# Kernel optimization log

Hardware: AMD Instinct MI355X
Metric: run time of the kernel (lower is better)

Reference implementation:

```python
import jax, jax.numpy as jnp
import numpy as np

B, N, K = 64, 1024, 16  # graphs per batch, nodes per graph, top-k (k=16 hardcoded in module)
EPS = 1e-20


def setup_inputs() -> dict:
    key = jax.random.key(0)
    ks = jax.random.split(key, 6)
    C = 128
    x = jax.random.normal(ks[0], (B * N, C), jnp.float32)
    pos = jax.random.normal(ks[1], (B * N, 3), jnp.float32)
    W1 = jax.random.normal(ks[2], (C, C), jnp.float32) / np.sqrt(C).astype(np.float32)
    b1 = jnp.zeros((C,), jnp.float32)
    gamma = jnp.ones((C,), jnp.float32)
    beta = jnp.zeros((C,), jnp.float32)
    W2 = jax.random.normal(ks[3], (C, 10), jnp.float32) / np.sqrt(C).astype(np.float32)
    b2 = jnp.zeros((10,), jnp.float32)
    t = jnp.ones((1,), jnp.float32)
    return dict(x=x, pos=pos, W1=W1, b1=b1, gamma=gamma, beta=beta, W2=W2, b2=b2, t=t)


def _edge_arrays(idx):
    # idx: (B, N, K) per-target top-k source node indices (graph-local)
    offs = (jnp.arange(B, dtype=jnp.int32) * N)[:, None, None]
    src = (idx + offs).reshape(-1)
    tgt = (jnp.broadcast_to(jnp.arange(N, dtype=jnp.int32)[None, :, None], (B, N, K)) + offs).reshape(-1)
    return jnp.stack([src, tgt])  # (2, B*N*K)


def _knn_edges(pos):
    # KNNGraph(k=16) on positions, loop=False (exclude self)
    p = pos.reshape(B, N, 3)
    d2 = jnp.sum((p[:, :, None, :] - p[:, None, :, :]) ** 2, axis=-1)  # (B,N,N)
    d2 = d2 + jnp.eye(N, dtype=d2.dtype) * 1e10
    _, idx = jax.lax.top_k(-d2, K)  # nearest K per node
    return _edge_arrays(idx)


def reference(x, pos, W1, b1, gamma, beta, W2, b2, t):
    key = jax.random.key(42)
    k1, k2 = jax.random.split(key)
    # tg MLP: lin -> batchnorm -> relu -> lin (training-mode batch stats over nodes)
    h = x @ W1 + b1
    mu = h.mean(axis=0)
    var = h.var(axis=0)
    h = (h - mu) / jnp.sqrt(var + 1e-5) * gamma + beta
    h = jax.nn.relu(h)
    emb = h @ W2 + b2  # (B*N, 10)
    emb = emb + jax.random.uniform(k1, emb.shape, emb.dtype) * 0.001
    e = emb.reshape(B, N, 10)
    # pairwise distances per graph (vectorized over the python loop in the original)
    diff = e[:, :, None, :] - e[:, None, :, :]  # (B,N,N,10)
    dist = jnp.linalg.norm(diff, axis=-1)  # (B,N,N)
    p = jnp.exp(-t[0] * dist ** 2)
    u = jax.random.uniform(k2, p.shape, p.dtype)
    gumbel = -jnp.log(-jnp.log(u + EPS) + EPS)
    noisy_logits = jnp.log(p + EPS) + gumbel
    # torch topk over dim=0 (sources) for each target column -> transpose then top_k on last axis
    vals, idx = jax.lax.top_k(jnp.swapaxes(noisy_logits, 1, 2), K)  # (B,N,K)
    vals = jax.nn.softmax(vals, axis=-1)
    vals = vals / vals.max(axis=-1, keepdims=True)
    soft_idx = _edge_arrays(idx)  # (2, B*N*K)
    knn_idx = _knn_edges(pos)
    edge_index = jnp.concatenate([soft_idx, knn_idx], axis=1)
    return vals.reshape(-1), soft_idx, edge_index
```

## Files before the change

### kernel.cpp

```cpp
#include <hip/hip_runtime.h>
#include <stdint.h>
#include <math.h>

#define BG 64
#define NG 1024
#define KK 16
#define CC 128
#define NNODE (BG * NG)
#define NSOFT (BG * NG * KK)
#define FEPS 1e-20f

__host__ __device__ __forceinline__ uint32_t rotl32u(uint32_t x, int r) {
  return (x << r) | (x >> (32 - r));
}

__host__ __device__ __forceinline__ void tf2x32(uint32_t k0, uint32_t k1,
                                                uint32_t x0, uint32_t x1,
                                                uint32_t &o0, uint32_t &o1) {
  uint32_t k2 = k0 ^ k1 ^ 0x1BD11BDAu;
  x0 += k0; x1 += k1;
#define TFR(r) { x0 += x1; x1 = rotl32u(x1, r); x1 ^= x0; }
  TFR(13) TFR(15) TFR(26) TFR(6)
  x0 += k1; x1 += k2 + 1u;
  TFR(17) TFR(29) TFR(16) TFR(24)
  x0 += k2; x1 += k0 + 2u;
  TFR(13) TFR(15) TFR(26) TFR(6)
  x0 += k0; x1 += k1 + 3u;
  TFR(17) TFR(29) TFR(16) TFR(24)
  x0 += k1; x1 += k2 + 4u;
  TFR(13) TFR(15) TFR(26) TFR(6)
  x0 += k2; x1 += k0 + 5u;
#undef TFR
  o0 = x0; o1 = x1;
}

__device__ __forceinline__ float jax_uniform01(uint32_t ka, uint32_t kb, uint32_t m) {
  uint32_t o0, o1;
  tf2x32(ka, kb, 0u, m, o0, o1);
  uint32_t bits = o0 ^ o1;
  float f = __uint_as_float((bits >> 9) | 0x3f800000u) - 1.0f;
  return fmaxf(f, 0.0f);
}

#define LDS_WAIT() asm volatile("s_waitcnt lgkmcnt(0)" ::: "memory")

__global__ __launch_bounds__(256) void k_gemm1(const float* __restrict__ x,
                                               const float* __restrict__ W1,
                                               const float* __restrict__ b1,
                                               float* __restrict__ h,
                                               float* __restrict__ p1,
                                               float* __restrict__ p2) {
  __shared__ __align__(16) float xs[64 * 128];
  const int t = threadIdx.x;
  const size_t blockBase = (size_t)blockIdx.x * (64 * 128);
  #pragma unroll
  for (int j = 0; j < 32; ++j) xs[t + j * 256] = x[blockBase + t + j * 256];
  __syncthreads();
  const int c = t & 127;
  const int rg = t >> 7;
  float acc[32];
  #pragma unroll
  for (int j = 0; j < 32; ++j) acc[j] = 0.f;
  const float* xrow = &xs[rg * 32 * 128];
  for (int k4 = 0; k4 < 128; k4 += 4) {
    const float w0 = W1[(size_t)(k4 + 0) * 128 + c];
    const float w1 = W1[(size_t)(k4 + 1) * 128 + c];
    const float w2 = W1[(size_t)(k4 + 2) * 128 + c];
    const float w3 = W1[(size_t)(k4 + 3) * 128 + c];
    #pragma unroll
    for (int j = 0; j < 32; ++j) {
      const float4 xv = *(const float4*)&xrow[j * 128 + k4];
      acc[j] = fmaf(xv.x, w0, acc[j]);
      acc[j] = fmaf(xv.y, w1, acc[j]);
      acc[j] = fmaf(xv.z, w2, acc[j]);
      acc[j] = fmaf(xv.w, w3, acc[j]);
    }
  }
  const float bb = b1[c];
  float s1 = 0.f, s2 = 0.f;
  #pragma unroll
  for (int j = 0; j < 32; ++j) {
    const float v = acc[j] + bb;
    h[blockBase + (size_t)(rg * 32 + j) * 128 + c] = v;
    s1 += v;
    s2 = fmaf(v, v, s2);
  }
  __syncthreads();
  float* r1 = xs;
  float* r2 = xs + 256;
  r1[rg * 128 + c] = s1;
  r2[rg * 128 + c] = s2;
  __syncthreads();
  if (t < 128) {
    p1[(size_t)t * 1024 + blockIdx.x] = r1[t] + r1[128 + t];
  } else {
    const int cc = t - 128;
    p2[(size_t)cc * 1024 + blockIdx.x] = r2[cc] + r2[128 + cc];
  }
}

__global__ __launch_bounds__(256) void k_bn_final(const float* __restrict__ p1,
                                                  const float* __restrict__ p2,
                                                  const float* __restrict__ gamma,
                                                  const float* __restrict__ beta,
                                                  float* __restrict__ scale,
                                                  float* __restrict__ shift) {
  const int c = blockIdx.x, t = threadIdx.x;
  const float* q1 = p1 + (size_t)c * 1024;
  const float* q2 = p2 + (size_t)c * 1024;
  float a1 = q1[t] + q1[t + 256] + q1[t + 512] + q1[t + 768];
  float a2 = q2[t] + q2[t + 256] + q2[t + 512] + q2[t + 768];
  __shared__ float r1[256], r2[256];
  r1[t] = a1; r2[t] = a2;
  __syncthreads();
  for (int o = 128; o > 0; o >>= 1) {
    if (t < o) { r1[t] += r1[t + o]; r2[t] += r2[t + o]; }
    __syncthreads();
  }
  if (t == 0) {
    const float mu = r1[0] * (1.0f / NNODE);
    float var = r2[0] * (1.0f / NNODE) - mu * mu;
    var = fmaxf(var, 0.f);
    const float sc = gamma[c] / sqrtf(var + 1e-5f);
    scale[c] = sc;
    shift[c] = beta[c] - mu * sc;
  }
}

__global__ __launch_bounds__(256) void k_emb(const float* __restrict__ h,
                                             const float* __restrict__ scale,
                                             const float* __restrict__ shift,
                                             const float* __restrict__ W2,
                                             const float* __restrict__ b2,
                                             float* __restrict__ e,
                                             uint32_t ka, uint32_t kb) {
  __shared__ __align__(16) float hn[64 * 132];
  const int t = threadIdx.x;
  const int rowBase = blockIdx.x * 64;
  {
    const int c = t & 127;
    const float sc = scale[c], sh = shift[c];
    #pragma unroll
    for (int j = 0; j < 32; ++j) {
      const int r = (t >> 7) + j * 2;
      const float v = fmaf(h[(size_t)(rowBase + r) * 128 + c], sc, sh);
      hn[r * 132 + c] = fmaxf(v, 0.f);
    }
  }
  __syncthreads();
  #pragma unroll
  for (int j = 0; j < 3; ++j) {
    const int o = t + j * 256;
    if (o < 640) {
      const int r = o / 10;
      const int col = o - r * 10;
      float acc = 0.f;
      for (int k4 = 0; k4 < 128; k4 += 4) {
        const float4 hv = *(const float4*)&hn[r * 132 + k4];
        acc = fmaf(hv.x, W2[(k4 + 0) * 10 + col], acc);
        acc = fmaf(hv.y, W2[(k4 + 1) * 10 + col], acc);
        acc = fmaf(hv.z, W2[(k4 + 2) * 10 + col], acc);
        acc = fmaf(hv.w, W2[(k4 + 3) * 10 + col], acc);
      }
      acc += b2[col];
      const uint32_t m = (uint32_t)(rowBase + r) * 10u + (uint32_t)col;
      const float u = jax_uniform01(ka, kb, m);
      e[(size_t)(rowBase + r) * 10 + col] = acc + u * 0.001f;
    }
  }
}

__global__ __launch_bounds__(1024, 4) void k_soft(const float* __restrict__ e,
                                                  const float* __restrict__ tsc,
                                                  float* __restrict__ out,
                                                  uint32_t ka, uint32_t kb) {
  __shared__ __align__(16) float2 els2[5 * NG];
  __shared__ float    cv[16][48];
  __shared__ int      cidx[16][48];
  __shared__ uint32_t cnt[16];
  __shared__ float    o16v[16][16];
  __shared__ int      o16i[16][16];

  const int t = threadIdx.x, lane = t & 63, w = t >> 6;
  const int node = blockIdx.x * 16 + w;
  const int b = blockIdx.x >> 6;
  const int jt = node & (NG - 1);
  const float negt = -tsc[0];
  const float* eg = e + (size_t)b * (NG * 10);

  if (lane == 0) cnt[w] = 0u;

  {
    const int s = t;
    const float2* rp = (const float2*)(eg + (size_t)s * 10);
    els2[0 * NG + s] = rp[0];
    els2[1 * NG + s] = rp[1];
    els2[2 * NG + s] = rp[2];
    els2[3 * NG + s] = rp[3];
    els2[4 * NG + s] = rp[4];
  }
  __syncthreads();

  float ej[10];
  #pragma unroll
  for (int p = 0; p < 5; ++p) {
    const float2 a = els2[p * NG + jt];
    ej[2 * p] = a.x; ej[2 * p + 1] = a.y;
  }

  float vv[16];
  const uint32_t mL = ((uint32_t)b << 20) + ((uint32_t)lane << 10) + (uint32_t)jt;
  const uint32_t kxa = ka, kxb = kb;
  const uint32_t kxc = ka ^ kb ^ 0x1BD11BDAu;

#define DIST(ACC, S) { \
    const float2 r0 = els2[0 * NG + (S)]; \
    const float2 r1 = els2[1 * NG + (S)]; \
    const float2 r2 = els2[2 * NG + (S)]; \
    const float2 r3 = els2[3 * NG + (S)]; \
    const float2 r4 = els2[4 * NG + (S)]; \
    float dd; \
    dd = ej[0] - r0.x; ACC = dd * dd; \
    dd = ej[1] - r0.y; ACC = fmaf(dd, dd, ACC); \
    dd = ej[2] - r1.x; ACC = fmaf(dd, dd, ACC); \
    dd = ej[3] - r1.y; ACC = fmaf(dd, dd, ACC); \
    dd = ej[4] - r2.x; ACC = fmaf(dd, dd, ACC); \
    dd = ej[5] - r2.y; ACC = fmaf(dd, dd, ACC); \
    dd = ej[6] - r3.x; ACC = fmaf(dd, dd, ACC); \
    dd = ej[7] - r3.y; ACC = fmaf(dd, dd, ACC); \
    dd = ej[8] - r4.x; ACC = fmaf(dd, dd, ACC); \
    dd = ej[9] - r4.y; ACC = fmaf(dd, dd, ACC); }

#define TFR4(r) { \
    xA0 += xA1; xA1 = rotl32u(xA1, r); xA1 ^= xA0; \
    xB0 += xB1; xB1 = rotl32u(xB1, r); xB1 ^= xB0; \
    xC0 += xC1; xC1 = rotl32u(xC1, r); xC1 ^= xC0; \
    xD0 += xD1; xD1 = rotl32u(xD1, r); xD1 ^= xD0; }
#define INJ4(A, B) { \
    xA0 += (A); xA1 += (B); \
    xB0 += (A); xB1 += (B); \
    xC0 += (A); xC1 += (B); \
    xD0 += (A); xD1 += (B); }

#define TAIL(ACC, X0, X1, ST) { \
    const uint32_t bits = (X0) ^ (X1); \
    float uu = __uint_as_float((bits >> 9) | 0x3f800000u) - 1.0f; \
    uu = fmaxf(uu, 0.0f); \
    const float dist = sqrtf(ACC); \
    const float d2 = dist * dist; \
    const float p = __expf(negt * d2); \
    const float li = __logf(uu + FEPS); \
    const float g = -__logf(FEPS - li); \
    vv[ST] = __logf(p + FEPS) + g; }

  #pragma unroll
  for (int g4 = 0; g4 < 4; ++g4) {
    const int sA = (g4 * 4 + 0) * 64 + lane;
    const int sB = (g4 * 4 + 1) * 64 + lane;
    const int sC = (g4 * 4 + 2) * 64 + lane;
    const int sD = (g4 * 4 + 3) * 64 + lane;
    float aA, aB, aC, aD;
    DIST(aA, sA)
    DIST(aB, sB)
    DIST(aC, sC)
    DIST(aD, sD)
    uint32_t xA0 = kxa, xA1 = (mL + (uint32_t)((g4 * 4 + 0) << 16)) + kxb;
    uint32_t xB0 = kxa, xB1 = (mL + (uint32_t)((g4 * 4 + 1) << 16)) + kxb;
    uint32_t xC0 = kxa, xC1 = (mL + (uint32_t)((g4 * 4 + 2) << 16)) + kxb;
    uint32_t xD0 = kxa, xD1 = (mL + (uint32_t)((g4 * 4 + 3) << 16)) + kxb;
    TFR4(13) TFR4(15) TFR4(26) TFR4(6)
    INJ4(kxb, kxc + 1u)
    TFR4(17) TFR4(29) TFR4(16) TFR4(24)
    INJ4(kxc, kxa + 2u)
    TFR4(13) TFR4(15) TFR4(26) TFR4(6)
    INJ4(kxa, kxb + 3u)
    TFR4(17) TFR4(29) TFR4(16) TFR4(24)
    INJ4(kxb, kxc + 4u)
    TFR4(13) TFR4(15) TFR4(26) TFR4(6)
    INJ4(kxc, kxa + 5u)
    TAIL(aA, xA0, xA1, g4 * 4 + 0)
    TAIL(aB, xB0, xB1, g4 * 4 + 1)
    TAIL(aC, xC0, xC1, g4 * 4 + 2)
    TAIL(aD, xD0, xD1, g4 * 4 + 3)
  }
#undef DIST
#undef TFR4
#undef INJ4
#undef TAIL

  float lo = -51.0f, hi = 17.0f;
  #pragma unroll 1
  for (int it = 0; it < 24; ++it) {
    const float mid = 0.5f * (lo + hi);
    int c = 0;
    #pragma unroll
    for (int st = 0; st < 16; ++st)
      c += (int)__popcll(__ballot(vv[st] >= mid));
    if (c >= 16) lo = mid; else hi = mid;
  }
  const float tau = lo;

  #pragma unroll
  for (int st = 0; st < 16; ++st) {
    if (vv[st] >= tau) {
      const uint32_t pos = atomicAdd(&cnt[w], 1u);
      if (pos < 48u) { cv[w][pos] = vv[st]; cidx[w][pos] = st * 64 + lane; }
    }
  }
  LDS_WAIT();

  int C = (int)cnt[w]; if (C > 48) C = 48;
  const float mvv = (lane < C) ? cv[w][lane] : 0.f;
  const int   mii = (lane < C) ? cidx[w][lane] : 0;
  int rank = 0;
  for (int j = 0; j < C; ++j) {
    const float vj = cv[w][j];
    const int ij = cidx[w][j];
    if (vj > mvv || (vj == mvv && ij < mii)) ++rank;
  }
  if (lane < C && rank < 16) { o16v[w][rank] = mvv; o16i[w][rank] = mii; }
  LDS_WAIT();

  if (lane < 16) {
    const float vq = o16v[w][lane];
    const float m0 = o16v[w][0];
    float uex = __expf(vq - m0);
    float ss = uex;
    #pragma unroll
    for (int off = 1; off < 16; off <<= 1) ss += __shfl_xor(ss, off, 16);
    const float u0 = __shfl(uex, 0, 16);
    const float s0v = u0 / ss;
    const float sv = uex / ss;
    const float o = sv / s0v;
    const size_t base = (size_t)node * KK + lane;
    const float tgtf = (float)node;
    const float srcf = (float)(b * NG + o16i[w][lane]);
    out[base] = o;
    out[(size_t)NSOFT + base] = srcf;
    out[2 * (size_t)NSOFT + base] = tgtf;
    out[3 * (size_t)NSOFT + base] = srcf;
    out[5 * (size_t)NSOFT + base] = tgtf;
  }
}

__global__ __launch_bounds__(1024, 4) void k_knn(const float* __restrict__ pos,
                                                 float* __restrict__ out) {
  __shared__ float    pls[3 * NG];
  __shared__ float    cv[16][48];
  __shared__ int      cidx[16][48];
  __shared__ uint32_t cnt[16];
  __shared__ int      o16i[16][16];

  const int t = threadIdx.x, lane = t & 63, w = t >> 6;
  const int node = blockIdx.x * 16 + w;
  const int b = blockIdx.x >> 6;
  const int it = node & (NG - 1);
  const float* pg = pos + (size_t)b * (NG * 3);

  if (lane == 0) cnt[w] = 0u;

  for (int f = t; f < 3072; f += 1024) {
    const int r = f / 3, d = f - r * 3;
    pls[d * NG + r] = pg[f];
  }
  __syncthreads();

  const float px = pls[0 * NG + it];
  const float py = pls[1 * NG + it];
  const float pz = pls[2 * NG + it];

  float vv[16];
  #pragma unroll
  for (int st = 0; st < 16; ++st) {
    const int s = st * 64 + lane;
    const float dx = px - pls[0 * NG + s];
    const float dy = py - pls[1 * NG + s];
    const float dz = pz - pls[2 * NG + s];
    float d2 = dx * dx;
    d2 = fmaf(dy, dy, d2);
    d2 = fmaf(dz, dz, d2);
    if (s == it) d2 += 1e10f;
    vv[st] = -d2;
  }

  float lo = -70.0f, hi = 1.0f;
  #pragma unroll 1
  for (int bs = 0; bs < 26; ++bs) {
    const float mid = 0.5f * (lo + hi);
    int c = 0;
    #pragma unroll
    for (int st = 0; st < 16; ++st)
      c += (int)__popcll(__ballot(vv[st] >= mid));
    if (c >= 16) lo = mid; else hi = mid;
  }
  const float tau = lo;

  #pragma unroll
  for (int st = 0; st < 16; ++st) {
    if (vv[st] >= tau) {
      const uint32_t pos = atomicAdd(&cnt[w], 1u);
      if (pos < 48u) { cv[w][pos] = vv[st]; cidx[w][pos] = st * 64 + lane; }
    }
  }
  LDS_WAIT();

  int C = (int)cnt[w]; if (C > 48) C = 48;
  const float mvv = (lane < C) ? cv[w][lane] : 0.f;
  const int   mii = (lane < C) ? cidx[w][lane] : 0;
  int rank = 0;
  for (int j = 0; j < C; ++j) {
    const float vj = cv[w][j];
    const int ij = cidx[w][j];
    if (vj > mvv || (vj == mvv && ij < mii)) ++rank;
  }
  if (lane < C && rank < 16) o16i[w][rank] = mii;
  LDS_WAIT();

  if (lane < 16) {
    const size_t base = (size_t)node * KK + lane;
    out[4 * (size_t)NSOFT + base] = (float)(b * NG + o16i[w][lane]);
    out[6 * (size_t)NSOFT + base] = (float)node;
  }
}

extern "C" void kernel_launch(void* const* d_in, const int* in_sizes, int n_in,
                              void* d_out, int out_size, void* d_ws, size_t ws_size,
                              hipStream_t stream) {
  const float* x     = (const float*)d_in[0];
  const float* pos   = (const float*)d_in[1];
  const float* W1    = (const float*)d_in[2];
  const float* b1    = (const float*)d_in[3];
  const float* gamma = (const float*)d_in[4];
  const float* beta  = (const float*)d_in[5];
  const float* W2    = (const float*)d_in[6];
  const float* b2    = (const float*)d_in[7];
  const float* t     = (const float*)d_in[8];
  float* out = (float*)d_out;

  float* ws    = (float*)d_ws;
  float* h     = ws;
  float* e     = h + (size_t)NNODE * CC;
  float* p1    = e + (size_t)NNODE * 10;
  float* p2    = p1 + 128 * 1024;
  float* scale = p2 + 128 * 1024;
  float* shift = scale + CC;

  uint32_t k1a, k1b, k2a, k2b;
  tf2x32(0u, 42u, 0u, 0u, k1a, k1b);
  tf2x32(0u, 42u, 0u, 1u, k2a, k2b);

  k_gemm1<<<dim3(NNODE / 64), dim3(256), 0, stream>>>(x, W1, b1, h, p1, p2);
  k_bn_final<<<dim3(CC), dim3(256), 0, stream>>>(p1, p2, gamma, beta, scale, shift);
  k_emb<<<dim3(NNODE / 64), dim3(256), 0, stream>>>(h, scale, shift, W2, b2, e, k1a, k1b);
  k_knn<<<dim3(NNODE / 16), dim3(1024), 0, stream>>>(pos, out);
  k_soft<<<dim3(NNODE / 16), dim3(1024), 0, stream>>>(e, t, out, k2a, k2b);
}
```

Measured before the change: 488.7 us.

## Store embeddings planar and read them from global/L2 instead of LDS in k_soft

```diff
diff --git a/kernel.cpp b/kernel.cpp
--- a/kernel.cpp
+++ b/kernel.cpp
@@ -132,9 +132,10 @@
                                              const float* __restrict__ shift,
                                              const float* __restrict__ W2,
                                              const float* __restrict__ b2,
-                                             float* __restrict__ e,
+                                             float2* __restrict__ et2,
                                              uint32_t ka, uint32_t kb) {
   __shared__ __align__(16) float hn[64 * 132];
+  __shared__ float et[64 * 10];
   const int t = threadIdx.x;
   const int rowBase = blockIdx.x * 64;
   {
@@ -165,46 +166,41 @@
       acc += b2[col];
       const uint32_t m = (uint32_t)(rowBase + r) * 10u + (uint32_t)col;
       const float u = jax_uniform01(ka, kb, m);
-      e[(size_t)(rowBase + r) * 10 + col] = acc + u * 0.001f;
+      et[r * 10 + col] = acc + u * 0.001f;
     }
   }
-}
-
-__global__ __launch_bounds__(1024, 4) void k_soft(const float* __restrict__ e,
-                                                  const float* __restrict__ tsc,
-                                                  float* __restrict__ out,
-                                                  uint32_t ka, uint32_t kb) {
-  __shared__ __align__(16) float2 els2[5 * NG];
-  __shared__ float    cv[16][48];
-  __shared__ int      cidx[16][48];
-  __shared__ uint32_t cnt[16];
-  __shared__ float    o16v[16][16];
-  __shared__ int      o16i[16][16];
+  __syncthreads();
+  if (t < 320) {
+    const int r = t & 63, p = t >> 6;
+    et2[(size_t)p * NNODE + rowBase + r] =
+        make_float2(et[r * 10 + 2 * p], et[r * 10 + 2 * p + 1]);
+  }
+}
+
+__global__ __launch_bounds__(256, 4) void k_soft(const float2* __restrict__ et2,
+                                                 const float* __restrict__ tsc,
+                                                 float* __restrict__ out,
+                                                 uint32_t ka, uint32_t kb) {
+  __shared__ float    cv[4][48];
+  __shared__ int      cidx[4][48];
+  __shared__ uint32_t cnt[4];
+  __shared__ float    o16v[4][16];
+  __shared__ int      o16i[4][16];
 
   const int t = threadIdx.x, lane = t & 63, w = t >> 6;
-  const int node = blockIdx.x * 16 + w;
-  const int b = blockIdx.x >> 6;
+  const int node = blockIdx.x * 4 + w;
+  const int b = node >> 10;
   const int jt = node & (NG - 1);
+  const int gb = b << 10;
   const float negt = -tsc[0];
-  const float* eg = e + (size_t)b * (NG * 10);
 
   if (lane == 0) cnt[w] = 0u;
-
-  {
-    const int s = t;
-    const float2* rp = (const float2*)(eg + (size_t)s * 10);
-    els2[0 * NG + s] = rp[0];
-    els2[1 * NG + s] = rp[1];
-    els2[2 * NG + s] = rp[2];
-    els2[3 * NG + s] = rp[3];
-    els2[4 * NG + s] = rp[4];
-  }
-  __syncthreads();
+  LDS_WAIT();
 
   float ej[10];
   #pragma unroll
   for (int p = 0; p < 5; ++p) {
-    const float2 a = els2[p * NG + jt];
+    const float2 a = et2[(size_t)p * NNODE + node];
     ej[2 * p] = a.x; ej[2 * p + 1] = a.y;
   }
 
@@ -214,11 +210,11 @@
   const uint32_t kxc = ka ^ kb ^ 0x1BD11BDAu;
 
 #define DIST(ACC, S) { \
-    const float2 r0 = els2[0 * NG + (S)]; \
-    const float2 r1 = els2[1 * NG + (S)]; \
-    const float2 r2 = els2[2 * NG + (S)]; \
-    const float2 r3 = els2[3 * NG + (S)]; \
-    const float2 r4 = els2[4 * NG + (S)]; \
+    const float2 r0 = et2[0 * (size_t)NNODE + gb + (S)]; \
+    const float2 r1 = et2[1 * (size_t)NNODE + gb + (S)]; \
+    const float2 r2 = et2[2 * (size_t)NNODE + gb + (S)]; \
+    const float2 r3 = et2[3 * (size_t)NNODE + gb + (S)]; \
+    const float2 r4 = et2[4 * (size_t)NNODE + gb + (S)]; \
     float dd; \
     dd = ej[0] - r0.x; ACC = dd * dd; \
     dd = ej[1] - r0.y; ACC = fmaf(dd, dd, ACC); \
@@ -309,14 +305,16 @@
   }
   LDS_WAIT();
 
-  int C = (int)cnt[w]; if (C > 48) C = 48;
+  const int C = min((int)cnt[w], 48);
   const float mvv = (lane < C) ? cv[w][lane] : 0.f;
   const int   mii = (lane < C) ? cidx[w][lane] : 0;
   int rank = 0;
-  for (int j = 0; j < C; ++j) {
+  #pragma unroll
+  for (int j = 0; j < 48; ++j) {
     const float vj = cv[w][j];
     const int ij = cidx[w][j];
-    if (vj > mvv || (vj == mvv && ij < mii)) ++rank;
+    const bool act = (j < C) && (vj > mvv || (vj == mvv && ij < mii));
+    rank += act ? 1 : 0;
   }
   if (lane < C && rank < 16) { o16v[w][rank] = mvv; o16i[w][rank] = mii; }
   LDS_WAIT();
@@ -334,7 +332,7 @@
     const float o = sv / s0v;
     const size_t base = (size_t)node * KK + lane;
     const float tgtf = (float)node;
-    const float srcf = (float)(b * NG + o16i[w][lane]);
+    const float srcf = (float)(gb + o16i[w][lane]);
     out[base] = o;
     out[(size_t)NSOFT + base] = srcf;
     out[2 * (size_t)NSOFT + base] = tgtf;
@@ -404,14 +402,16 @@
   }
   LDS_WAIT();
 
-  int C = (int)cnt[w]; if (C > 48) C = 48;
+  const int C = min((int)cnt[w], 48);
   const float mvv = (lane < C) ? cv[w][lane] : 0.f;
   const int   mii = (lane < C) ? cidx[w][lane] : 0;
   int rank = 0;
-  for (int j = 0; j < C; ++j) {
+  #pragma unroll
+  for (int j = 0; j < 48; ++j) {
     const float vj = cv[w][j];
     const int ij = cidx[w][j];
-    if (vj > mvv || (vj == mvv && ij < mii)) ++rank;
+    const bool act = (j < C) && (vj > mvv || (vj == mvv && ij < mii));
+    rank += act ? 1 : 0;
   }
   if (lane < C && rank < 16) o16i[w][rank] = mii;
   LDS_WAIT();
@@ -439,8 +439,8 @@
 
   float* ws    = (float*)d_ws;
   float* h     = ws;
-  float* e     = h + (size_t)NNODE * CC;
-  float* p1    = e + (size_t)NNODE * 10;
+  float2* et2  = (float2*)(h + (size_t)NNODE * CC);
+  float* p1    = (float*)(et2 + 5 * (size_t)NNODE);
   float* p2    = p1 + 128 * 1024;
   float* scale = p2 + 128 * 1024;
   float* shift = scale + CC;
@@ -451,7 +451,7 @@
 
   k_gemm1<<<dim3(NNODE / 64), dim3(256), 0, stream>>>(x, W1, b1, h, p1, p2);
   k_bn_final<<<dim3(CC), dim3(256), 0, stream>>>(p1, p2, gamma, beta, scale, shift);
-  k_emb<<<dim3(NNODE / 64), dim3(256), 0, stream>>>(h, scale, shift, W2, b2, e, k1a, k1b);
+  k_emb<<<dim3(NNODE / 64), dim3(256), 0, stream>>>(h, scale, shift, W2, b2, et2, k1a, k1b);
   k_knn<<<dim3(NNODE / 16), dim3(1024), 0, stream>>>(pos, out);
-  k_soft<<<dim3(NNODE / 16), dim3(1024), 0, stream>>>(e, t, out, k2a, k2b);
-}
+  k_soft<<<dim3(NNODE / 4), dim3(256), 0, stream>>>(et2, t, out, k2a, k2b);
+}
```

Result: slower. 513.6 us (+5.1%).
